# Performance work log

Measured on AMD Instinct MI355X. Metric: run time of the kernel, lower is better.

The kernel has to match this reference:

```python
import jax, jax.numpy as jnp
import numpy as np

N, T, P = 1024, 512, 2
H = 128  # hidden_channels == lstm_input_channels == num_fc_concat == 128


def _lin(k, out_dim, in_dim):
    # torch nn.Linear default init: U(-1/sqrt(in), 1/sqrt(in))
    b = 1.0 / np.sqrt(in_dim)
    return jax.random.uniform(k, (out_dim, in_dim), minval=-b, maxval=b, dtype=jnp.float32)


def setup_inputs() -> dict:
    key = jax.random.key(0)
    ks = jax.random.split(key, 12)
    bnd = lambda k, sh, inn: jax.random.uniform(k, sh, minval=-1.0/np.sqrt(inn), maxval=1.0/np.sqrt(inn), dtype=jnp.float32)
    return {
        "x": jax.random.normal(ks[0], (N, T, P), dtype=jnp.float32),
        "enc1_w": _lin(ks[1], 128, 2),
        "enc1_b": bnd(ks[2], (128,), 2),
        "enc2_w": _lin(ks[3], H, 128),
        "enc2_b": bnd(ks[4], (H,), 128),
        "w_ih": _lin(ks[5], 4 * H, H),   # LSTMCell weight_ih, gate order i,f,g,o; bias=False
        "w_hh": _lin(ks[6], 4 * H, H),
        "dec1_w": _lin(ks[7], H, 2 * H),
        "dec1_b": bnd(ks[8], (H,), 2 * H),
        "dec2_w": _lin(ks[9], 1, H),
        "dec2_b": bnd(ks[10], (1,), H),
    }


def reference(x, enc1_w, enc1_b, enc2_w, enc2_b, w_ih, w_hh, dec1_w, dec1_b, dec2_w, dec2_b):
    n = x.shape[0]
    # Encoder MLP applied to every (n, t) position at once: (N,T,2) -> (N,T,H)
    feat = jax.nn.relu(jnp.einsum('ntp,hp->nth', x, enc1_w) + enc1_b)
    feat = jnp.einsum('nth,oh->nto', feat, enc2_w) + enc2_b
    feat_t = jnp.swapaxes(feat, 0, 1)  # (T,N,H)

    def step(carry, xt):
        h, c = carry
        gates = xt @ w_ih.T + h @ w_hh.T  # (N, 4H)
        i, f, g, o = jnp.split(gates, 4, axis=-1)
        c = jax.nn.sigmoid(f) * c + jax.nn.sigmoid(i) * jnp.tanh(g)
        h = jax.nn.sigmoid(o) * jnp.tanh(c)
        return (h, c), h

    init = (jnp.zeros((n, H), dtype=x.dtype), jnp.zeros((n, H), dtype=x.dtype))
    # Shared LSTMCell weights run forward and backward over time
    _, h_fw = jax.lax.scan(step, init, feat_t)            # (T,N,H)
    _, h_bw_rev = jax.lax.scan(step, init, feat_t[::-1])  # (T,N,H) over reversed time
    h_bw = h_bw_rev[::-1]

    final = jax.nn.relu(jnp.concatenate([h_fw, h_bw], axis=-1))  # (T,N,2H)
    q = jax.nn.relu(jnp.einsum('tnk,hk->tnh', final, dec1_w) + dec1_b)
    q = jnp.einsum('tnh,oh->tno', q, dec2_w) + dec2_b  # (T,N,1)
    return jnp.swapaxes(q[..., 0], 0, 1)  # (N,T)
```

## Files before the change

### kernel.cpp

```cpp
#include <hip/hip_runtime.h>
#include <hip/hip_fp16.h>
#include <stdint.h>


#define TN 512
#define NB 1024

typedef __attribute__((ext_vector_type(8))) _Float16 f16x8;
typedef __attribute__((ext_vector_type(4))) float f32x4;

#define MFMA16(a,b,c) __builtin_amdgcn_mfma_f32_16x16x32_f16(a,b,c,0,0,0)
#define RCP(x) __builtin_amdgcn_rcpf(x)

__device__ __forceinline__ f16x8 cvt_frag(const float* p){
  f32x4 a = *(const f32x4*)p;
  f32x4 b = *(const f32x4*)(p+4);
  f16x8 h;
  h[0]=(_Float16)a[0]; h[1]=(_Float16)a[1]; h[2]=(_Float16)a[2]; h[3]=(_Float16)a[3];
  h[4]=(_Float16)b[0]; h[5]=(_Float16)b[1]; h[6]=(_Float16)b[2]; h[7]=(_Float16)b[3];
  return h;
}

__device__ __forceinline__ unsigned short f2h(float f){
  return __half_as_ushort(__float2half(f));
}

__global__ __launch_bounds__(256) void enc_kernel(
    const float* __restrict__ x,  const float* __restrict__ e1w,
    const float* __restrict__ e1b,const float* __restrict__ e2w,
    const float* __restrict__ e2b,
    unsigned short* __restrict__ featA, unsigned short* __restrict__ featB)
{
  __shared__ float xs[64][2];
  __shared__ unsigned int A32[64][68];
  __shared__ unsigned short A2[64][136];
  int tid = threadIdx.x;
  long rowbase = (long)blockIdx.x * 64;
  if (tid < 128){
    int i = tid >> 1, cc = tid & 1;
    long row = rowbase + i;
    int t = (int)(row >> 10), n = (int)(row & 1023);
    xs[i][cc] = x[((size_t)n * TN + t) * 2 + cc];
  }
  int w4 = tid >> 6, lane = tid & 63, lq = lane >> 4, lr = lane & 15;
  f16x8 Bf[2][4];
  float b2v[2];
  #pragma unroll
  for (int nt2 = 0; nt2 < 2; nt2++){
    int col = (w4*2 + nt2)*16 + lr;
    b2v[nt2] = e2b[col];
    #pragma unroll
    for (int ks = 0; ks < 4; ks++)
      Bf[nt2][ks] = cvt_frag(e2w + col*128 + ks*32 + lq*8);
  }
  int q = tid >> 6, dp = tid & 63;
  float w00 = e1w[4*dp], w01 = e1w[4*dp+1], w10 = e1w[4*dp+2], w11 = e1w[4*dp+3];
  float b0 = e1b[2*dp], b1 = e1b[2*dp+1];
  __syncthreads();
  #pragma unroll
  for (int rr = 0; rr < 16; rr++){
    int r = q*16 + rr;
    float x0 = xs[r][0], x1 = xs[r][1];
    float v0 = fmaxf(w00*x0 + w01*x1 + b0, 0.f);
    float v1 = fmaxf(w10*x0 + w11*x1 + b1, 0.f);
    A32[r][dp] = (unsigned int)f2h(v0) | ((unsigned int)f2h(v1) << 16);
  }
  __syncthreads();
  #pragma unroll
  for (int Mt = 0; Mt < 4; Mt++){
    f16x8 ah[4];
    #pragma unroll
    for (int ks = 0; ks < 4; ks++)
      ah[ks] = *(const f16x8*)((const unsigned short*)&A32[Mt*16+lr][0] + ks*32 + lq*8);
    f32x4 acc0 = {0.f,0.f,0.f,0.f}, acc1 = {0.f,0.f,0.f,0.f};
    #pragma unroll
    for (int ks = 0; ks < 4; ks++){
      acc0 = MFMA16(ah[ks], Bf[0][ks], acc0);
      acc1 = MFMA16(ah[ks], Bf[1][ks], acc1);
    }
    #pragma unroll
    for (int r = 0; r < 4; r++){
      int lrow = Mt*16 + lq*4 + r;
      A2[lrow][(w4*2+0)*16 + lr] = f2h(acc0[r] + b2v[0]);
      A2[lrow][(w4*2+1)*16 + lr] = f2h(acc1[r] + b2v[1]);
    }
  }
  __syncthreads();
  #pragma unroll
  for (int it = 0; it < 4; it++){
    int idx = it*256 + tid;
    int row = idx >> 4, qq = idx & 15;
    uint4 v = *(const uint4*)&A2[row][qq*8];
    *(uint4*)(featA + ((size_t)(rowbase + row))*128 + qq*8) = v;
    *(uint4*)(featB + ((size_t)(rowbase + row))*128 + qq*8) = v;
  }
}

#define LSTM_STEP(P, PFC, PFN) do { \
    f16x8 ah[4]; \
    _Pragma("unroll") \
    for (int ks = 0; ks < 4; ks++) ah[ks] = *(const f16x8*)&hbS[P][smr][ks*32 + lq*8]; \
    _Pragma("unroll") \
    for (int ks = 0; ks < 4; ks++) PFN[ks] = *(const uint4*)(fpp + ks*32); \
    fpp += dstep; \
    f32x4 acc[4]; \
    _Pragma("unroll") \
    for (int G = 0; G < 4; G++) acc[G] = MFMA16(*(const f16x8*)&PFC[0], wg[G][0], zero4); \
    _Pragma("unroll") \
    for (int ks = 1; ks < 4; ks++){ \
      _Pragma("unroll") \
      for (int G = 0; G < 4; G++) acc[G] = MFMA16(*(const f16x8*)&PFC[ks], wg[G][ks], acc[G]); \
    } \
    _Pragma("unroll") \
    for (int ks = 0; ks < 4; ks++){ \
      _Pragma("unroll") \
      for (int G = 0; G < 4; G++) acc[G] = MFMA16(ah[ks], wg[G][4+ks], acc[G]); \
    } \
    _Pragma("unroll") \
    for (int r = 0; r < 2; r++){ \
      float iv = acc[0][r], fv = acc[1][r], gv = acc[2][r], ov = acc[3][r]; \
      float si = RCP(1.f + __expf(-iv)); \
      float sf = RCP(1.f + __expf(-fv)); \
      float so = RCP(1.f + __expf(-ov)); \
      float tg = 1.f - 2.f*RCP(__expf(2.f*gv) + 1.f); \
      c[r] = sf*c[r] + si*tg; \
      float tc = 1.f - 2.f*RCP(__expf(2.f*c[r]) + 1.f); \
      float hv = so*tc; \
      unsigned short hh = f2h(hv); \
      hbS[(P)^1][lq*2+r][w*16 + lr] = hh; \
      op[r*128] = (hv > 0.f) ? hh : (unsigned short)0; \
    } \
    op += dstep; \
    __syncthreads(); \
  } while(0)

__global__ __launch_bounds__(512, 2) void lstm_kernel(
    unsigned short* bufA, unsigned short* bufB,
    const float* __restrict__ wih, const float* __restrict__ whh)
{
  __shared__ __align__(16) unsigned short hbS[2][8][136];
  int tid = threadIdx.x, b = blockIdx.x;
  int dir = b >> 7, n0 = (b & 127) << 3;
  int w = tid >> 6, lane = tid & 63, lq = lane >> 4, lr = lane & 15;
  unsigned short* buf = dir ? bufB : bufA;

  f16x8 wg[4][8];
  #pragma unroll
  for (int G = 0; G < 4; G++){
    int gate = G*128 + w*16 + lr;
    #pragma unroll
    for (int ks = 0; ks < 8; ks++){
      const float* src = (ks < 4) ? (wih + (size_t)gate*128 + ks*32 + lq*8)
                                  : (whh + (size_t)gate*128 + (ks-4)*32 + lq*8);
      wg[G][ks] = cvt_frag(src);
    }
  }

  for (int i = tid; i < 1088; i += 512) ((unsigned int*)hbS)[i] = 0u;

  int smr = ((lr >> 2) << 1) | (lr & 1);
  float c[2] = {0.f, 0.f};
  const f32x4 zero4 = {0.f, 0.f, 0.f, 0.f};
  int t0 = dir ? (TN-1) : 0;
  long dstep = dir ? -(long)(NB*128) : (long)(NB*128);

  const unsigned short* fpp = buf + ((size_t)t0*NB + n0 + smr)*128 + lq*8;
  uint4 pfA[4], pfB[4];
  #pragma unroll
  for (int ks = 0; ks < 4; ks++) pfA[ks] = *(const uint4*)(fpp + ks*32);
  fpp += dstep;

  unsigned short* op = buf + ((size_t)t0*NB + n0 + lq*2)*128 + (w*16 + lr);
  __syncthreads();

  for (int s2 = 0; s2 < TN/2; s2++){
    LSTM_STEP(0, pfA, pfB);
    LSTM_STEP(1, pfB, pfA);
  }
}

__global__ __launch_bounds__(256) void dec_kernel(
    const unsigned short* __restrict__ hfw, const unsigned short* __restrict__ hbw,
    const float* __restrict__ d1w, const float* __restrict__ d1b,
    const float* __restrict__ d2w, const float* __restrict__ d2b,
    float* __restrict__ out)
{
  __shared__ unsigned short A[64][264];
  __shared__ float partial[4][64];
  int tid = threadIdx.x;
  int w4 = tid >> 6, lane = tid & 63, lq = lane >> 4, lr = lane & 15;
  f16x8 Bf[2][8];
  float b1v[2], w2v[2];
  #pragma unroll
  for (int nt2 = 0; nt2 < 2; nt2++){
    int col = (w4*2 + nt2)*16 + lr;
    b1v[nt2] = d1b[col];
    w2v[nt2] = d2w[col];
    #pragma unroll
    for (int ks = 0; ks < 8; ks++)
      Bf[nt2][ks] = cvt_frag(d1w + col*256 + ks*32 + lq*8);
  }
  float b2s = d2b[0];

  for (int ch = 0; ch < 4; ch++){
    long rowbase = (long)blockIdx.x * 256 + ch * 64;
    #pragma unroll
    for (int u = 0; u < 8; u++){
      int chunk = u*256 + tid;
      int row = chunk >> 5, seg = chunk & 31;
      const unsigned short* src = (seg < 16)
          ? (hfw + ((size_t)(rowbase + row))*128 + seg*8)
          : (hbw + ((size_t)(rowbase + row))*128 + (seg-16)*8);
      *(uint4*)&A[row][seg*8] = *(const uint4*)src;
    }
    __syncthreads();
    #pragma unroll
    for (int Mt = 0; Mt < 4; Mt++){
      f16x8 ah[8];
      #pragma unroll
      for (int ks = 0; ks < 8; ks++)
        ah[ks] = *(const f16x8*)&A[Mt*16+lr][ks*32 + lq*8];
      f32x4 acc0 = {0.f,0.f,0.f,0.f}, acc1 = {0.f,0.f,0.f,0.f};
      #pragma unroll
      for (int ks = 0; ks < 8; ks++){
        acc0 = MFMA16(ah[ks], Bf[0][ks], acc0);
        acc1 = MFMA16(ah[ks], Bf[1][ks], acc1);
      }
      #pragma unroll
      for (int r = 0; r < 4; r++){
        float p = fmaxf(acc0[r] + b1v[0], 0.f) * w2v[0]
                + fmaxf(acc1[r] + b1v[1], 0.f) * w2v[1];
        p += __shfl_xor(p, 1);
        p += __shfl_xor(p, 2);
        p += __shfl_xor(p, 4);
        p += __shfl_xor(p, 8);
        if (lr == 0) partial[w4][Mt*16 + lq*4 + r] = p;
      }
    }
    __syncthreads();
    if (tid < 64){
      long row = rowbase + tid;
      int t = (int)(row >> 10), n = (int)(row & 1023);
      out[(size_t)n*TN + t] = partial[0][tid] + partial[1][tid]
                            + partial[2][tid] + partial[3][tid] + b2s;
    }
  }
}

extern "C" void kernel_launch(void* const* d_in, const int* in_sizes, int n_in,
                              void* d_out, int out_size, void* d_ws, size_t ws_size,
                              hipStream_t stream)
{
  const float* x   = (const float*)d_in[0];
  const float* e1w = (const float*)d_in[1];
  const float* e1b = (const float*)d_in[2];
  const float* e2w = (const float*)d_in[3];
  const float* e2b = (const float*)d_in[4];
  const float* wih = (const float*)d_in[5];
  const float* whh = (const float*)d_in[6];
  const float* d1w = (const float*)d_in[7];
  const float* d1b = (const float*)d_in[8];
  const float* d2w = (const float*)d_in[9];
  const float* d2b = (const float*)d_in[10];
  float* out = (float*)d_out;

  if (ws_size < ((size_t)256 << 20)) return;

  char* ws = (char*)d_ws;
  unsigned short* bufA = (unsigned short*)ws;
  unsigned short* bufB = (unsigned short*)(ws + (((size_t)128) << 20));

  hipLaunchKernelGGL(enc_kernel, dim3(8192), dim3(256), 0, stream, x, e1w, e1b, e2w, e2b, bufA, bufB);
  hipLaunchKernelGGL(lstm_kernel, dim3(256), dim3(512), 0, stream, bufA, bufB, wih, whh);
  hipLaunchKernelGGL(dec_kernel, dim3(2048), dim3(256), 0, stream, bufA, bufB, d1w, d1b, d2w, d2b, out);
}
```

Before: 631.0 us.

## Pack two timesteps into each MFMA tile to share input-projection work in LSTM

The LSTM kernel now fills the 16 MFMA rows with 8 batch rows times two consecutive timesteps. One set of input-projection MFMAs therefore covers both steps of a window. The recurrent h@W_hh contribution is added in two passes, each reading a zero-padded shared-memory h buffer so that only the matching timestep rows receive the term. This removes a quarter of the MFMAs per step pair and halves the feature prefetch count. The cost is that the recurrent MFMAs now do half-wasted work on zero rows, and the shared h buffer is twice as large.

New measurement: 619.6 us (median of 2 runs). About the same (-1.8%).

```diff
diff --git a/kernel.cpp b/kernel.cpp
--- a/kernel.cpp
+++ b/kernel.cpp
@@ -96,86 +96,110 @@
   }
 }
 
-#define LSTM_STEP(P, PFC, PFN) do { \
-    f16x8 ah[4]; \
-    _Pragma("unroll") \
-    for (int ks = 0; ks < 4; ks++) ah[ks] = *(const f16x8*)&hbS[P][smr][ks*32 + lq*8]; \
+#define LSTM_EW(RA, RB, ZW, RO) do { \
+    float iv0=acc[0][RA], fv0=acc[1][RA], gv0=acc[2][RA], ov0=acc[3][RA]; \
+    float si0 = RCP(1.f + __expf(-iv0)); \
+    float sf0 = RCP(1.f + __expf(-fv0)); \
+    float so0 = RCP(1.f + __expf(-ov0)); \
+    float tg0 = 1.f - 2.f*RCP(__expf(2.f*gv0) + 1.f); \
+    c[0] = sf0*c[0] + si0*tg0; \
+    float tc0 = 1.f - 2.f*RCP(__expf(2.f*c[0]) + 1.f); \
+    float hv0 = so0*tc0; \
+    float iv1=acc[0][RB], fv1=acc[1][RB], gv1=acc[2][RB], ov1=acc[3][RB]; \
+    float si1 = RCP(1.f + __expf(-iv1)); \
+    float sf1 = RCP(1.f + __expf(-fv1)); \
+    float so1 = RCP(1.f + __expf(-ov1)); \
+    float tg1 = 1.f - 2.f*RCP(__expf(2.f*gv1) + 1.f); \
+    c[1] = sf1*c[1] + si1*tg1; \
+    float tc1 = 1.f - 2.f*RCP(__expf(2.f*c[1]) + 1.f); \
+    float hv1 = so1*tc1; \
+    unsigned short hh0 = f2h(hv0), hh1 = f2h(hv1); \
+    ZW[4*lq + (RO)][w*16 + lr]     = hh0; \
+    ZW[4*lq + 2 + (RO)][w*16 + lr] = hh1; \
+    op[0]   = (hv0 > 0.f) ? hh0 : (unsigned short)0; \
+    op[128] = (hv1 > 0.f) ? hh1 : (unsigned short)0; \
+    op += dstep; \
+  } while(0)
+
+#define LSTM_WINDOW(PFC, PFN) do { \
     _Pragma("unroll") \
     for (int ks = 0; ks < 4; ks++) PFN[ks] = *(const uint4*)(fpp + ks*32); \
-    fpp += dstep; \
+    fpp += 2*dstep; \
     f32x4 acc[4]; \
     _Pragma("unroll") \
-    for (int G = 0; G < 4; G++) acc[G] = MFMA16(*(const f16x8*)&PFC[0], wg[G][0], zero4); \
+    for (int G = 0; G < 4; G++) acc[G] = MFMA16(*(const f16x8*)&PFC[0], wf[G][0], zero4); \
     _Pragma("unroll") \
     for (int ks = 1; ks < 4; ks++){ \
       _Pragma("unroll") \
-      for (int G = 0; G < 4; G++) acc[G] = MFMA16(*(const f16x8*)&PFC[ks], wg[G][ks], acc[G]); \
+      for (int G = 0; G < 4; G++) acc[G] = MFMA16(*(const f16x8*)&PFC[ks], wf[G][ks], acc[G]); \
     } \
-    _Pragma("unroll") \
-    for (int ks = 0; ks < 4; ks++){ \
-      _Pragma("unroll") \
-      for (int G = 0; G < 4; G++) acc[G] = MFMA16(ah[ks], wg[G][4+ks], acc[G]); \
+    {  \
+      f16x8 ah[4]; \
+      _Pragma("unroll") \
+      for (int ks = 0; ks < 4; ks++) ah[ks] = *(const f16x8*)&Z[0][lr][ks*32 + lq*8]; \
+      _Pragma("unroll") \
+      for (int ks = 0; ks < 4; ks++){ \
+        _Pragma("unroll") \
+        for (int G = 0; G < 4; G++) acc[G] = MFMA16(ah[ks], wh[G][ks], acc[G]); \
+      } \
     } \
-    _Pragma("unroll") \
-    for (int r = 0; r < 2; r++){ \
-      float iv = acc[0][r], fv = acc[1][r], gv = acc[2][r], ov = acc[3][r]; \
-      float si = RCP(1.f + __expf(-iv)); \
-      float sf = RCP(1.f + __expf(-fv)); \
-      float so = RCP(1.f + __expf(-ov)); \
-      float tg = 1.f - 2.f*RCP(__expf(2.f*gv) + 1.f); \
-      c[r] = sf*c[r] + si*tg; \
-      float tc = 1.f - 2.f*RCP(__expf(2.f*c[r]) + 1.f); \
-      float hv = so*tc; \
-      unsigned short hh = f2h(hv); \
-      hbS[(P)^1][lq*2+r][w*16 + lr] = hh; \
-      op[r*128] = (hv > 0.f) ? hh : (unsigned short)0; \
+    LSTM_EW(0, 2, Z[1], 1);    \
+    __syncthreads();           \
+    {  \
+      f16x8 ah[4]; \
+      _Pragma("unroll") \
+      for (int ks = 0; ks < 4; ks++) ah[ks] = *(const f16x8*)&Z[1][lr][ks*32 + lq*8]; \
+      _Pragma("unroll") \
+      for (int ks = 0; ks < 4; ks++){ \
+        _Pragma("unroll") \
+        for (int G = 0; G < 4; G++) acc[G] = MFMA16(ah[ks], wh[G][ks], acc[G]); \
+      } \
     } \
-    op += dstep; \
-    __syncthreads(); \
+    LSTM_EW(1, 3, Z[0], 0);    \
+    __syncthreads();           \
   } while(0)
 
 __global__ __launch_bounds__(512, 2) void lstm_kernel(
     unsigned short* bufA, unsigned short* bufB,
     const float* __restrict__ wih, const float* __restrict__ whh)
 {
-  __shared__ __align__(16) unsigned short hbS[2][8][136];
+  __shared__ __align__(16) unsigned short Z[2][16][136];
   int tid = threadIdx.x, b = blockIdx.x;
   int dir = b >> 7, n0 = (b & 127) << 3;
   int w = tid >> 6, lane = tid & 63, lq = lane >> 4, lr = lane & 15;
   unsigned short* buf = dir ? bufB : bufA;
 
-  f16x8 wg[4][8];
+  f16x8 wf[4][4], wh[4][4];
   #pragma unroll
   for (int G = 0; G < 4; G++){
     int gate = G*128 + w*16 + lr;
     #pragma unroll
-    for (int ks = 0; ks < 8; ks++){
-      const float* src = (ks < 4) ? (wih + (size_t)gate*128 + ks*32 + lq*8)
-                                  : (whh + (size_t)gate*128 + (ks-4)*32 + lq*8);
-      wg[G][ks] = cvt_frag(src);
-    }
-  }
-
-  for (int i = tid; i < 1088; i += 512) ((unsigned int*)hbS)[i] = 0u;
-
-  int smr = ((lr >> 2) << 1) | (lr & 1);
+    for (int ks = 0; ks < 4; ks++){
+      wf[G][ks] = cvt_frag(wih + (size_t)gate*128 + ks*32 + lq*8);
+      wh[G][ks] = cvt_frag(whh + (size_t)gate*128 + ks*32 + lq*8);
+    }
+  }
+
+  for (int i = tid; i < 2176; i += 512) ((unsigned int*)Z)[i] = 0u;
+
   float c[2] = {0.f, 0.f};
   const f32x4 zero4 = {0.f, 0.f, 0.f, 0.f};
   int t0 = dir ? (TN-1) : 0;
   long dstep = dir ? -(long)(NB*128) : (long)(NB*128);
 
-  const unsigned short* fpp = buf + ((size_t)t0*NB + n0 + smr)*128 + lq*8;
+  const unsigned short* fpp = buf + ((size_t)t0*NB + n0 + (lr >> 1))*128
+                            + (long)(lr & 1)*dstep + lq*8;
   uint4 pfA[4], pfB[4];
   #pragma unroll
   for (int ks = 0; ks < 4; ks++) pfA[ks] = *(const uint4*)(fpp + ks*32);
-  fpp += dstep;
+  fpp += 2*dstep;
 
   unsigned short* op = buf + ((size_t)t0*NB + n0 + lq*2)*128 + (w*16 + lr);
   __syncthreads();
 
-  for (int s2 = 0; s2 < TN/2; s2++){
-    LSTM_STEP(0, pfA, pfB);
-    LSTM_STEP(1, pfB, pfA);
+  for (int wd = 0; wd < 128; wd++){
+    LSTM_WINDOW(pfA, pfB);
+    LSTM_WINDOW(pfB, pfA);
   }
 }
 
```

## Batch input projection over 4 timesteps per MFMA tile and halve rows per block

Applied to the files above, without the earlier changes.

The LSTM kernel now gives each block 4 sequences instead of 8 and launches 512 blocks. Each 16-row MFMA tile of the input projection packs 4 timesteps × 4 sequences, so the x·W_ih product is computed once per 4-step window. The recurrent h·W_hh product still runs every step from a rotating 4-slot shared buffer, and only the relevant accumulator row is consumed. This removes redundant input-projection MFMAs and spreads the work over more blocks. In exchange, 12 of the 16 rows in each recurrent MFMA are wasted, and launch bounds of 4 blocks per CU put pressure on registers.

Measured after the change: 1.558 ms. 2.47x slower.

```diff
diff --git a/kernel.cpp b/kernel.cpp
--- a/kernel.cpp
+++ b/kernel.cpp
@@ -96,86 +96,91 @@
   }
 }
 
-#define LSTM_STEP(P, PFC, PFN) do { \
+#define HPASS(J) do { \
     f16x8 ah[4]; \
     _Pragma("unroll") \
-    for (int ks = 0; ks < 4; ks++) ah[ks] = *(const f16x8*)&hbS[P][smr][ks*32 + lq*8]; \
-    _Pragma("unroll") \
-    for (int ks = 0; ks < 4; ks++) PFN[ks] = *(const uint4*)(fpp + ks*32); \
-    fpp += dstep; \
-    f32x4 acc[4]; \
-    _Pragma("unroll") \
-    for (int G = 0; G < 4; G++) acc[G] = MFMA16(*(const f16x8*)&PFC[0], wg[G][0], zero4); \
-    _Pragma("unroll") \
-    for (int ks = 1; ks < 4; ks++){ \
-      _Pragma("unroll") \
-      for (int G = 0; G < 4; G++) acc[G] = MFMA16(*(const f16x8*)&PFC[ks], wg[G][ks], acc[G]); \
-    } \
+    for (int ks = 0; ks < 4; ks++) ah[ks] = *(const f16x8*)&Z[J][lr][ks*32 + lq*8]; \
     _Pragma("unroll") \
     for (int ks = 0; ks < 4; ks++){ \
       _Pragma("unroll") \
-      for (int G = 0; G < 4; G++) acc[G] = MFMA16(ah[ks], wg[G][4+ks], acc[G]); \
+      for (int G = 0; G < 4; G++) acc[G] = MFMA16(ah[ks], wh[G][ks], acc[G]); \
     } \
-    _Pragma("unroll") \
-    for (int r = 0; r < 2; r++){ \
-      float iv = acc[0][r], fv = acc[1][r], gv = acc[2][r], ov = acc[3][r]; \
+    { \
+      float iv = acc[0][J], fv = acc[1][J], gv = acc[2][J], ov = acc[3][J]; \
       float si = RCP(1.f + __expf(-iv)); \
       float sf = RCP(1.f + __expf(-fv)); \
       float so = RCP(1.f + __expf(-ov)); \
       float tg = 1.f - 2.f*RCP(__expf(2.f*gv) + 1.f); \
-      c[r] = sf*c[r] + si*tg; \
-      float tc = 1.f - 2.f*RCP(__expf(2.f*c[r]) + 1.f); \
+      cst = sf*cst + si*tg; \
+      float tc = 1.f - 2.f*RCP(__expf(2.f*cst) + 1.f); \
       float hv = so*tc; \
       unsigned short hh = f2h(hv); \
-      hbS[(P)^1][lq*2+r][w*16 + lr] = hh; \
-      op[r*128] = (hv > 0.f) ? hh : (unsigned short)0; \
+      Z[((J)+1)&3][4*lq + (((J)+1)&3)][w*16 + lr] = hh; \
+      *op = (hv > 0.f) ? hh : (unsigned short)0; \
+      op += dstep; \
     } \
-    op += dstep; \
     __syncthreads(); \
   } while(0)
 
-__global__ __launch_bounds__(512, 2) void lstm_kernel(
+#define LSTM_WINDOW(PFC, PFN) do { \
+    _Pragma("unroll") \
+    for (int ks = 0; ks < 4; ks++) PFN[ks] = *(const uint4*)(fpp + ks*32); \
+    fpp += 4*dstep; \
+    f32x4 acc[4]; \
+    _Pragma("unroll") \
+    for (int G = 0; G < 4; G++) acc[G] = MFMA16(*(const f16x8*)&PFC[0], wf[G][0], zero4); \
+    _Pragma("unroll") \
+    for (int ks = 1; ks < 4; ks++){ \
+      _Pragma("unroll") \
+      for (int G = 0; G < 4; G++) acc[G] = MFMA16(*(const f16x8*)&PFC[ks], wf[G][ks], acc[G]); \
+    } \
+    HPASS(0); \
+    HPASS(1); \
+    HPASS(2); \
+    HPASS(3); \
+  } while(0)
+
+__global__ __launch_bounds__(512, 4) void lstm_kernel(
     unsigned short* bufA, unsigned short* bufB,
     const float* __restrict__ wih, const float* __restrict__ whh)
 {
-  __shared__ __align__(16) unsigned short hbS[2][8][136];
+  __shared__ __align__(16) unsigned short Z[4][16][136];
   int tid = threadIdx.x, b = blockIdx.x;
-  int dir = b >> 7, n0 = (b & 127) << 3;
+  int dir = b & 1, n0 = (b >> 1) << 2;
   int w = tid >> 6, lane = tid & 63, lq = lane >> 4, lr = lane & 15;
   unsigned short* buf = dir ? bufB : bufA;
 
-  f16x8 wg[4][8];
+  f16x8 wf[4][4], wh[4][4];
   #pragma unroll
   for (int G = 0; G < 4; G++){
     int gate = G*128 + w*16 + lr;
     #pragma unroll
-    for (int ks = 0; ks < 8; ks++){
-      const float* src = (ks < 4) ? (wih + (size_t)gate*128 + ks*32 + lq*8)
-                                  : (whh + (size_t)gate*128 + (ks-4)*32 + lq*8);
-      wg[G][ks] = cvt_frag(src);
-    }
-  }
-
-  for (int i = tid; i < 1088; i += 512) ((unsigned int*)hbS)[i] = 0u;
-
-  int smr = ((lr >> 2) << 1) | (lr & 1);
-  float c[2] = {0.f, 0.f};
+    for (int ks = 0; ks < 4; ks++){
+      wf[G][ks] = cvt_frag(wih + (size_t)gate*128 + ks*32 + lq*8);
+      wh[G][ks] = cvt_frag(whh + (size_t)gate*128 + ks*32 + lq*8);
+    }
+  }
+
+  for (int i = tid; i < 4352; i += 512) ((unsigned int*)Z)[i] = 0u;
+
+  float cst = 0.f;
   const f32x4 zero4 = {0.f, 0.f, 0.f, 0.f};
   int t0 = dir ? (TN-1) : 0;
   long dstep = dir ? -(long)(NB*128) : (long)(NB*128);
 
-  const unsigned short* fpp = buf + ((size_t)t0*NB + n0 + smr)*128 + lq*8;
+  const unsigned short* fpp = buf + ((size_t)t0*NB + n0 + (lr >> 2))*128
+                            + (long)(lr & 3)*dstep + lq*8;
   uint4 pfA[4], pfB[4];
   #pragma unroll
   for (int ks = 0; ks < 4; ks++) pfA[ks] = *(const uint4*)(fpp + ks*32);
-  fpp += dstep;
-
-  unsigned short* op = buf + ((size_t)t0*NB + n0 + lq*2)*128 + (w*16 + lr);
-  __syncthreads();
-
-  for (int s2 = 0; s2 < TN/2; s2++){
-    LSTM_STEP(0, pfA, pfB);
-    LSTM_STEP(1, pfB, pfA);
+  fpp += 4*dstep;
+
+  unsigned short* op = buf + ((size_t)t0*NB + n0 + lq)*128 + (w*16 + lr);
+  __syncthreads();
+
+  for (int wd = 0; wd < 64; wd++){
+    LSTM_WINDOW(pfA, pfB);
+    LSTM_WINDOW(pfB, pfA);
   }
 }
 
@@ -271,6 +276,6 @@
   unsigned short* bufB = (unsigned short*)(ws + (((size_t)128) << 20));
 
   hipLaunchKernelGGL(enc_kernel, dim3(8192), dim3(256), 0, stream, x, e1w, e1b, e2w, e2b, bufA, bufB);
-  hipLaunchKernelGGL(lstm_kernel, dim3(256), dim3(512), 0, stream, bufA, bufB, wih, whh);
+  hipLaunchKernelGGL(lstm_kernel, dim3(512), dim3(512), 0, stream, bufA, bufB, wih, whh);
   hipLaunchKernelGGL(dec_kernel, dim3(2048), dim3(256), 0, stream, bufA, bufB, d1w, d1b, d2w, d2b, out);
 }
```
